# Kernel tuning notes

Measured on AMD Instinct MI355X. Metric: run time of the kernel, lower is better.

## Reference

```python
import jax, jax.numpy as jnp
import numpy as np

HIDDEN = 128
HEADS = 8
HEAD_DIM = HIDDEN // HEADS  # 16
N_NODE_TYPES = 3
N_EDGE_TYPES = 5
N_SRC = 50000
N_DST = 50000
N_EDGES = 800000
SCALE = float(np.sqrt(HEAD_DIM))


def setup_inputs() -> dict:
    key = jax.random.key(0)
    ks = jax.random.split(key, 12)
    lim = 1.0 / np.sqrt(HIDDEN)  # torch Linear default init range
    # xavier_uniform for [H, d, d] relation tensors: gain*sqrt(6/(fan_in+fan_out))
    xav = float(np.sqrt(6.0 / (HEAD_DIM + HEAD_DIM)))
    return {
        "x_src": jax.random.normal(ks[0], (N_SRC, HIDDEN), jnp.float32),
        "x_dst": jax.random.normal(ks[1], (N_DST, HIDDEN), jnp.float32),
        "edge_index": jax.random.randint(ks[2], (2, N_EDGES), 0, N_DST),
        "src_type": 0,
        "edge_type": 1,
        "dst_type": 2,
        "k_w": jax.random.uniform(ks[3], (N_NODE_TYPES, HIDDEN, HIDDEN), jnp.float32, -lim, lim),
        "k_b": jax.random.uniform(ks[4], (N_NODE_TYPES, HIDDEN), jnp.float32, -lim, lim),
        "q_w": jax.random.uniform(ks[5], (N_NODE_TYPES, HIDDEN, HIDDEN), jnp.float32, -lim, lim),
        "q_b": jax.random.uniform(ks[6], (N_NODE_TYPES, HIDDEN), jnp.float32, -lim, lim),
        "v_w": jax.random.uniform(ks[7], (N_NODE_TYPES, HIDDEN, HIDDEN), jnp.float32, -lim, lim),
        "v_b": jax.random.uniform(ks[8], (N_NODE_TYPES, HIDDEN), jnp.float32, -lim, lim),
        "relation_att": jax.random.uniform(ks[9], (N_EDGE_TYPES, HEADS, HEAD_DIM, HEAD_DIM), jnp.float32, -xav, xav),
        "relation_msg": jax.random.uniform(ks[10], (N_EDGE_TYPES, HEADS, HEAD_DIM, HEAD_DIM), jnp.float32, -xav, xav),
        "relation_pri": jnp.ones((N_EDGE_TYPES, HEADS), jnp.float32),
    }


def reference(x_src, x_dst, edge_index, src_type, edge_type, dst_type,
              k_w, k_b, q_w, q_b, v_w, v_b,
              relation_att, relation_msg, relation_pri):
    n_dst = x_dst.shape[0]
    # relation-specific node projections (torch Linear: x @ W.T + b)
    k = (x_src @ k_w[src_type].T + k_b[src_type]).reshape(-1, HEADS, HEAD_DIM)
    v = (x_src @ v_w[src_type].T + v_b[src_type]).reshape(-1, HEADS, HEAD_DIM)
    q = (x_dst @ q_w[dst_type].T + q_b[dst_type]).reshape(-1, HEADS, HEAD_DIM)

    src_idx, dst_idx = edge_index[0], edge_index[1]
    # gather + per-edge relation matmul: [E, H, d]
    k_edge = jnp.einsum('ehi,hio->eho', k[src_idx], relation_att[edge_type])
    att = (k_edge * q[dst_idx]).sum(-1) / SCALE + relation_pri[edge_type][None, :]  # [E, H]

    # segmented softmax over incoming edges per dst node.
    # torch scatter_reduce amax starts from a zero-initialized buffer -> max(0, seg_max)
    seg_max = jnp.maximum(jax.ops.segment_max(att, dst_idx, num_segments=n_dst), 0.0)
    att_exp = jnp.exp(att - seg_max[dst_idx])
    seg_sum = jnp.maximum(jax.ops.segment_sum(att_exp, dst_idx, num_segments=n_dst), 1e-8)
    att_n = att_exp / seg_sum[dst_idx]  # [E, H]

    # messages + weighted scatter-add aggregation
    msg = jnp.einsum('ehi,hio->eho', v[src_idx], relation_msg[edge_type])  # [E, H, d]
    out = jax.ops.segment_sum(att_n[..., None] * msg, dst_idx, num_segments=n_dst)
    return out.reshape(n_dst, HIDDEN)
```

## Files before the change

### kernel.cpp

```cpp
#include <hip/hip_runtime.h>

#define HIDDEN 128
#define HEADS 8
#define HDIM 16
#define BW 64

typedef unsigned int uint;
typedef unsigned short ushort;
typedef __attribute__((ext_vector_type(8))) short bfrag;
typedef __attribute__((ext_vector_type(4))) float f32x4;

__device__ inline ushort f2bf(float f) {
    uint u = __float_as_uint(f);
    uint r = ((u >> 16) & 1u) + 0x7fffu;
    return (ushort)((u + r) >> 16);
}
__device__ inline float bf2f(ushort h) { return __uint_as_float((uint)h << 16); }
__device__ inline float bfl(uint u) { return __uint_as_float(u << 16); }
__device__ inline float bfh(uint u) { return __uint_as_float(u & 0xffff0000u); }

__device__ inline int frag_addr(int k, int n) {
    int ks = k >> 5, kr = k & 31, nt = n >> 4;
    int lane = ((kr >> 3) << 4) | (n & 15);
    return ((ks * 8 + nt) * 64 + lane) * 8 + (kr & 7);
}

__global__ void k1a_weights_zero(
    const float* __restrict__ k_w, const float* __restrict__ k_b,
    const float* __restrict__ q_w, const float* __restrict__ q_b,
    const float* __restrict__ v_w, const float* __restrict__ v_b,
    const float* __restrict__ r_att, const float* __restrict__ r_msg,
    const int* __restrict__ stp, const int* __restrict__ etp, const int* __restrict__ dtp,
    ushort* __restrict__ WkHi, ushort* __restrict__ WvHi, ushort* __restrict__ WqHi,
    float* __restrict__ bk, float* __restrict__ bv, float* __restrict__ bq,
    int* __restrict__ deg, int n_dst)
{
    int idx = blockIdx.x * 256 + threadIdx.x;
    for (int i = idx; i < n_dst; i += 64 * 256) deg[i] = 0;

    int st = stp[0], et = etp[0], dt = dtp[0];
    int c = idx >> 7, j = idx & 127;
    int h = j >> 4, o = j & 15;
    const float* kw = k_w + (size_t)st * HIDDEN * HIDDEN;
    const float* vw = v_w + (size_t)st * HIDDEN * HIDDEN;
    const float* ra = r_att + (size_t)et * HEADS * HDIM * HDIM + h * HDIM * HDIM + o;
    const float* rm = r_msg + (size_t)et * HEADS * HDIM * HDIM + h * HDIM * HDIM + o;
    float sk = 0.f, sv = 0.f;
#pragma unroll
    for (int i = 0; i < HDIM; ++i) {
        sk += kw[(h * HDIM + i) * HIDDEN + c] * ra[i * HDIM];
        sv += vw[(h * HDIM + i) * HIDDEN + c] * rm[i * HDIM];
    }
    float sq = q_w[(size_t)dt * HIDDEN * HIDDEN + (size_t)j * HIDDEN + c];
    int fa = frag_addr(c, j);
    WkHi[fa] = f2bf(sk);
    WvHi[fa] = f2bf(sv);
    WqHi[fa] = f2bf(sq);
    if (idx < HIDDEN) {
        float sb = 0.f, sbv = 0.f;
#pragma unroll
        for (int i = 0; i < HDIM; ++i) {
            sb  += k_b[st * HIDDEN + h * HDIM + i] * ra[i * HDIM];
            sbv += v_b[st * HIDDEN + h * HDIM + i] * rm[i * HDIM];
        }
        bk[idx] = sb;
        bv[idx] = sbv;
        bq[idx] = q_b[dt * HIDDEN + idx];
    }
}

__global__ __launch_bounds__(256, 5) void k1b_proj_countfill(
    const float* __restrict__ x_src, const float* __restrict__ x_dst,
    const ushort* __restrict__ WkHi, const ushort* __restrict__ WvHi,
    const ushort* __restrict__ WqHi,
    const float* __restrict__ bk, const float* __restrict__ bv,
    const float* __restrict__ bq,
    ushort* __restrict__ kr16, ushort* __restrict__ vm16,
    float* __restrict__ qout, int n_src, int n_dst, int nsb, int nprojb,
    const int* __restrict__ ei, int* __restrict__ deg,
    ushort* __restrict__ bucket, int n_edges, int nfb)
{
    __shared__ float xs[32 * 132];
    int blk = blockIdx.x;

    if ((blk % 5) == 4) {
        int fidx = blk / 5;
        if (fidx >= nfb) return;
        int t = fidx * 256 + threadIdx.x;
        int base = t * 4;
        if (base >= n_edges) return;
        if (base + 3 < n_edges) {
            int4 ss = *(const int4*)(ei + base);
            int4 dd = *(const int4*)(ei + n_edges + base);
            int r0 = atomicAdd(&deg[dd.x], 1); if (r0 < BW) bucket[(size_t)dd.x * BW + r0] = (ushort)ss.x;
            int r1 = atomicAdd(&deg[dd.y], 1); if (r1 < BW) bucket[(size_t)dd.y * BW + r1] = (ushort)ss.y;
            int r2 = atomicAdd(&deg[dd.z], 1); if (r2 < BW) bucket[(size_t)dd.z * BW + r2] = (ushort)ss.z;
            int r3 = atomicAdd(&deg[dd.w], 1); if (r3 < BW) bucket[(size_t)dd.w * BW + r3] = (ushort)ss.w;
        } else {
            for (int e = base; e < n_edges; ++e) {
                int d = ei[n_edges + e];
                int r = atomicAdd(&deg[d], 1);
                if (r < BW) bucket[(size_t)d * BW + r] = (ushort)ei[e];
            }
        }
        return;
    }

    int pidx = blk - blk / 5;
    if (pidx >= nprojb) return;
    int is_src = (pidx < nsb) ? 1 : 0;
    int brow0 = (is_src ? pidx : pidx - nsb) * 32;
    int n = is_src ? n_src : n_dst;
    const float* x = is_src ? x_src : x_dst;
    int t = threadIdx.x;

    {
        const float4* xg = (const float4*)x;
#pragma unroll
        for (int k = 0; k < 4; ++k) {
            int fi = t + k * 256;
            int r = fi >> 5, c4 = fi & 31;
            int row = brow0 + r;
            float4 v = xg[(size_t)(row < n ? row : n - 1) * 32 + c4];
            *(float4*)&xs[r * 132 + c4 * 4] = v;
        }
    }
    __syncthreads();

    int w = t >> 6, l = t & 63;
    int l15 = l & 15, kgrp = l >> 4;
    int nthalf = w & 1;
    int rtile = w >> 1;
    int rowbase = brow0 + rtile * 16;

    bfrag ahi[4];
#pragma unroll
    for (int ks = 0; ks < 4; ++ks) {
        const float* xr = &xs[(rtile * 16 + l15) * 132 + ks * 32 + kgrp * 8];
        float4 x0 = *(const float4*)xr;
        float4 x1 = *(const float4*)(xr + 4);
        float xv[8] = {x0.x, x0.y, x0.z, x0.w, x1.x, x1.y, x1.z, x1.w};
#pragma unroll
        for (int b = 0; b < 8; ++b) {
            ahi[ks][b] = (short)f2bf(xv[b]);
        }
    }

    if (is_src) {
        const bfrag* Fk = (const bfrag*)WkHi;
        const bfrag* Fv = (const bfrag*)WvHi;
#pragma unroll
        for (int nt4 = 0; nt4 < 4; ++nt4) {
            int nt = nthalf * 4 + nt4;
            f32x4 ak = (f32x4){0.f, 0.f, 0.f, 0.f};
            f32x4 av = (f32x4){0.f, 0.f, 0.f, 0.f};
#pragma unroll
            for (int ks = 0; ks < 4; ++ks) {
                int fi = (ks * 8 + nt) * 64 + l;
                bfrag wk = Fk[fi], wv = Fv[fi];
                ak = __builtin_amdgcn_mfma_f32_16x16x32_bf16(ahi[ks], wk, ak, 0, 0, 0);
                av = __builtin_amdgcn_mfma_f32_16x16x32_bf16(ahi[ks], wv, av, 0, 0, 0);
            }
            int col = nt * 16 + l15;
            float bkc = bk[col], bvc = bv[col];
#pragma unroll
            for (int r = 0; r < 4; ++r) {
                int row = rowbase + kgrp * 4 + r;
                if (row < n) {
                    kr16[(size_t)row * HIDDEN + col] = f2bf(ak[r] + bkc);
                    vm16[(size_t)row * HIDDEN + col] = f2bf(av[r] + bvc);
                }
            }
        }
    } else {
        const bfrag* Fq = (const bfrag*)WqHi;
#pragma unroll
        for (int nt4 = 0; nt4 < 4; ++nt4) {
            int nt = nthalf * 4 + nt4;
            f32x4 aq = (f32x4){0.f, 0.f, 0.f, 0.f};
#pragma unroll
            for (int ks = 0; ks < 4; ++ks) {
                int fi = (ks * 8 + nt) * 64 + l;
                bfrag wq = Fq[fi];
                aq = __builtin_amdgcn_mfma_f32_16x16x32_bf16(ahi[ks], wq, aq, 0, 0, 0);
            }
            int col = nt * 16 + l15;
            float bqc = bq[col];
#pragma unroll
            for (int r = 0; r < 4; ++r) {
                int row = rowbase + kgrp * 4 + r;
                if (row < n) qout[(size_t)row * HIDDEN + col] = aq[r] + bqc;
            }
        }
    }
}

__global__ void fused_gather_kernel(const ushort* __restrict__ kr16,
                                    const ushort* __restrict__ vm16,
                                    const float* __restrict__ q,
                                    const float* __restrict__ pri,
                                    const int* __restrict__ etp,
                                    const int* __restrict__ deg,
                                    const ushort* __restrict__ bucket,
                                    float* __restrict__ out, int n_dst)
{
    int wave = (int)((blockIdx.x * 256 + threadIdx.x) >> 6);
    int l = threadIdx.x & 63;
    if (wave >= n_dst) return;
    int d = wave;
    int h = l >> 3;
    int e = l & 7;
    int len = deg[d]; if (len > BW) len = BW;
    const ushort* buck = bucket + (size_t)d * BW;

    const float4* qp = (const float4*)(q + (size_t)d * HIDDEN + h * HDIM);
    float4 q0 = qp[0], q1 = qp[1], q2 = qp[2], q3 = qp[3];
    float prih = pri[etp[0] * HEADS + h];

    float m = 0.0f;
    float ssum = 0.0f;
    float accx = 0.0f, accy = 0.0f;

    for (int i0 = 0; i0 < len; i0 += 16) {
        int ieA = i0 + e, ieB = i0 + 8 + e;
        bool vA = ieA < len, vB = ieB < len;
        int sA = buck[vA ? ieA : 0];
        int sB = buck[vB ? ieB : 0];

        const uint4* kpA = (const uint4*)(kr16 + (size_t)sA * HIDDEN + h * HDIM);
        const uint4* kpB = (const uint4*)(kr16 + (size_t)sB * HIDDEN + h * HDIM);
        uint4 kaA = kpA[0], kbA = kpA[1];
        uint4 kaB = kpB[0], kbB = kpB[1];

        float dotA =
            bfl(kaA.x) * q0.x + bfh(kaA.x) * q0.y + bfl(kaA.y) * q0.z + bfh(kaA.y) * q0.w +
            bfl(kaA.z) * q1.x + bfh(kaA.z) * q1.y + bfl(kaA.w) * q1.z + bfh(kaA.w) * q1.w +
            bfl(kbA.x) * q2.x + bfh(kbA.x) * q2.y + bfl(kbA.y) * q2.z + bfh(kbA.y) * q2.w +
            bfl(kbA.z) * q3.x + bfh(kbA.z) * q3.y + bfl(kbA.w) * q3.z + bfh(kbA.w) * q3.w;
        float dotB =
            bfl(kaB.x) * q0.x + bfh(kaB.x) * q0.y + bfl(kaB.y) * q0.z + bfh(kaB.y) * q0.w +
            bfl(kaB.z) * q1.x + bfh(kaB.z) * q1.y + bfl(kaB.w) * q1.z + bfh(kaB.w) * q1.w +
            bfl(kbB.x) * q2.x + bfh(kbB.x) * q2.y + bfl(kbB.y) * q2.z + bfh(kbB.y) * q2.w +
            bfl(kbB.z) * q3.x + bfh(kbB.z) * q3.y + bfl(kbB.w) * q3.z + bfh(kbB.w) * q3.w;

        float aA = vA ? (dotA * 0.25f + prih) : -3.0e38f;
        float aB = vB ? (dotB * 0.25f + prih) : -3.0e38f;

        float pm = fmaxf(aA, aB);
        pm = fmaxf(pm, __shfl_xor(pm, 1));
        pm = fmaxf(pm, __shfl_xor(pm, 2));
        pm = fmaxf(pm, __shfl_xor(pm, 4));
        float mnew = fmaxf(m, pm);
        float c = __expf(m - mnew);
        float wA = vA ? __expf(aA - mnew) : 0.0f;
        float wB = vB ? __expf(aB - mnew) : 0.0f;
        float S = wA + wB;
        S += __shfl_xor(S, 1);
        S += __shfl_xor(S, 2);
        S += __shfl_xor(S, 4);
        ssum = ssum * c + S;
        accx *= c;
        accy *= c;
        m = mnew;

#pragma unroll
        for (int ee = 0; ee < 8; ++ee) {
            int se = __shfl(sA, ee);
            float we = __shfl(wA, (l & 56) | ee);
            uint vv = *(const uint*)(vm16 + (size_t)se * HIDDEN + 2 * l);
            accx += we * bfl(vv);
            accy += we * bfh(vv);
        }
        if (i0 + 8 < len) {
#pragma unroll
            for (int ee = 0; ee < 8; ++ee) {
                int se = __shfl(sB, ee);
                float we = __shfl(wB, (l & 56) | ee);
                uint vv = *(const uint*)(vm16 + (size_t)se * HIDDEN + 2 * l);
                accx += we * bfl(vv);
                accy += we * bfh(vv);
            }
        }
    }

    float inv = 1.0f / fmaxf(ssum, 1e-8f);
    float2 o; o.x = accx * inv; o.y = accy * inv;
    *(float2*)(out + (size_t)d * HIDDEN + 2 * l) = o;
}

extern "C" void kernel_launch(void* const* d_in, const int* in_sizes, int n_in,
                              void* d_out, int out_size, void* d_ws, size_t ws_size,
                              hipStream_t stream)
{
    const float* x_src = (const float*)d_in[0];
    const float* x_dst = (const float*)d_in[1];
    const int*   ei    = (const int*)d_in[2];
    const int*   stp   = (const int*)d_in[3];
    const int*   etp   = (const int*)d_in[4];
    const int*   dtp   = (const int*)d_in[5];
    const float* k_w   = (const float*)d_in[6];
    const float* k_b   = (const float*)d_in[7];
    const float* q_w   = (const float*)d_in[8];
    const float* q_b   = (const float*)d_in[9];
    const float* v_w   = (const float*)d_in[10];
    const float* v_b   = (const float*)d_in[11];
    const float* r_att = (const float*)d_in[12];
    const float* r_msg = (const float*)d_in[13];
    const float* r_pri = (const float*)d_in[14];

    int n_src   = in_sizes[0] / HIDDEN;
    int n_dst   = in_sizes[1] / HIDDEN;
    int n_edges = in_sizes[2] / 2;
    float* out = (float*)d_out;

    char* p = (char*)d_ws;
    ushort* kr16 = (ushort*)p;            p += (size_t)n_src * HIDDEN * sizeof(ushort);
    ushort* vm16 = (ushort*)p;            p += (size_t)n_src * HIDDEN * sizeof(ushort);
    float*  qv   = (float*)p;             p += (size_t)n_dst * HIDDEN * sizeof(float);
    ushort* bucket = (ushort*)p;          p += (size_t)n_dst * BW * sizeof(ushort);
    int* deg     = (int*)p;               p += (size_t)n_dst * sizeof(int);
    float* bk = (float*)p;                p += HIDDEN * sizeof(float);
    float* bv = (float*)p;                p += HIDDEN * sizeof(float);
    float* bq = (float*)p;                p += HIDDEN * sizeof(float);
    ushort* WkHi = (ushort*)p;            p += HIDDEN * HIDDEN * sizeof(ushort);
    ushort* WvHi = (ushort*)p;            p += HIDDEN * HIDDEN * sizeof(ushort);
    ushort* WqHi = (ushort*)p;            p += HIDDEN * HIDDEN * sizeof(ushort);

    k1a_weights_zero<<<64, 256, 0, stream>>>(
        k_w, k_b, q_w, q_b, v_w, v_b, r_att, r_msg, stp, etp, dtp,
        WkHi, WvHi, WqHi, bk, bv, bq, deg, n_dst);

    int nsb = (n_src + 31) / 32;
    int ndb = (n_dst + 31) / 32;
    int nprojb = nsb + ndb;
    int nfb = (n_edges / 4 + 256) / 256;
    int grid1 = 5 * nfb;
    int grid2 = ((nprojb + 3) / 4) * 5;
    int grid = grid1 > grid2 ? grid1 : grid2;
    k1b_proj_countfill<<<grid, 256, 0, stream>>>(
        x_src, x_dst, WkHi, WvHi, WqHi, bk, bv, bq,
        kr16, vm16, qv, n_src, n_dst, nsb, nprojb,
        ei, deg, bucket, n_edges, nfb);

    fused_gather_kernel<<<(int)(((size_t)n_dst * 64 + 255) / 256), 256, 0, stream>>>(
        kr16, vm16, qv, r_pri, etp, deg, bucket, out, n_dst);
}
```

Baseline: 128.4 us.

## Process two destination nodes per wave and rebalance edge-fill interleaving

The gather kernel now has each wavefront handle two destination nodes at once, interleaving their key and value gathers so more independent memory loads are in flight per wave. The grid is halved to match. Separately, the projection/count-fill kernel switches from a 4:1 projection-to-fill block interleave with four edges per thread to a 1:1 interleave with one edge per thread. The aim is to hide gather latency and spread the atomic fill work more evenly, at the cost of more registers per thread, lower occupancy, and wasted iterations when the two nodes have different degrees.

```diff
diff --git a/kernel.cpp b/kernel.cpp
--- a/kernel.cpp
+++ b/kernel.cpp
@@ -83,30 +83,19 @@
     __shared__ float xs[32 * 132];
     int blk = blockIdx.x;
 
-    if ((blk % 5) == 4) {
-        int fidx = blk / 5;
+    if (blk & 1) {
+        int fidx = blk >> 1;
         if (fidx >= nfb) return;
-        int t = fidx * 256 + threadIdx.x;
-        int base = t * 4;
-        if (base >= n_edges) return;
-        if (base + 3 < n_edges) {
-            int4 ss = *(const int4*)(ei + base);
-            int4 dd = *(const int4*)(ei + n_edges + base);
-            int r0 = atomicAdd(&deg[dd.x], 1); if (r0 < BW) bucket[(size_t)dd.x * BW + r0] = (ushort)ss.x;
-            int r1 = atomicAdd(&deg[dd.y], 1); if (r1 < BW) bucket[(size_t)dd.y * BW + r1] = (ushort)ss.y;
-            int r2 = atomicAdd(&deg[dd.z], 1); if (r2 < BW) bucket[(size_t)dd.z * BW + r2] = (ushort)ss.z;
-            int r3 = atomicAdd(&deg[dd.w], 1); if (r3 < BW) bucket[(size_t)dd.w * BW + r3] = (ushort)ss.w;
-        } else {
-            for (int e = base; e < n_edges; ++e) {
-                int d = ei[n_edges + e];
-                int r = atomicAdd(&deg[d], 1);
-                if (r < BW) bucket[(size_t)d * BW + r] = (ushort)ei[e];
-            }
-        }
+        int e = fidx * 256 + threadIdx.x;
+        if (e >= n_edges) return;
+        int s = ei[e];
+        int d = ei[n_edges + e];
+        int r = atomicAdd(&deg[d], 1);
+        if (r < BW) bucket[(size_t)d * BW + r] = (ushort)s;
         return;
     }
 
-    int pidx = blk - blk / 5;
+    int pidx = blk >> 1;
     if (pidx >= nprojb) return;
     int is_src = (pidx < nsb) ? 1 : 0;
     int brow0 = (is_src ? pidx : pidx - nsb) * 32;
@@ -206,86 +195,162 @@
 {
     int wave = (int)((blockIdx.x * 256 + threadIdx.x) >> 6);
     int l = threadIdx.x & 63;
-    if (wave >= n_dst) return;
-    int d = wave;
+    int d0 = wave * 2;
+    if (d0 >= n_dst) return;
+    int d1 = d0 + 1;
+    bool has1 = d1 < n_dst;
     int h = l >> 3;
     int e = l & 7;
-    int len = deg[d]; if (len > BW) len = BW;
-    const ushort* buck = bucket + (size_t)d * BW;
-
-    const float4* qp = (const float4*)(q + (size_t)d * HIDDEN + h * HDIM);
-    float4 q0 = qp[0], q1 = qp[1], q2 = qp[2], q3 = qp[3];
+
+    int len0 = deg[d0]; if (len0 > BW) len0 = BW;
+    int len1 = has1 ? deg[d1] : 0; if (len1 > BW) len1 = BW;
+    const ushort* buck0 = bucket + (size_t)d0 * BW;
+    const ushort* buck1 = bucket + (size_t)d1 * BW;
+
+    const float4* qp0 = (const float4*)(q + (size_t)d0 * HIDDEN + h * HDIM);
+    float4 q00 = qp0[0], q01 = qp0[1], q02 = qp0[2], q03 = qp0[3];
+    const float4* qp1 = (const float4*)(q + (size_t)(has1 ? d1 : d0) * HIDDEN + h * HDIM);
+    float4 q10 = qp1[0], q11 = qp1[1], q12 = qp1[2], q13 = qp1[3];
+
     float prih = pri[etp[0] * HEADS + h];
 
-    float m = 0.0f;
-    float ssum = 0.0f;
-    float accx = 0.0f, accy = 0.0f;
-
-    for (int i0 = 0; i0 < len; i0 += 16) {
+    float m0 = 0.0f, ss0 = 0.0f, ax0 = 0.0f, ay0 = 0.0f;
+    float m1 = 0.0f, ss1 = 0.0f, ax1 = 0.0f, ay1 = 0.0f;
+
+    int lenmax = len0 > len1 ? len0 : len1;
+    for (int i0 = 0; i0 < lenmax; i0 += 16) {
         int ieA = i0 + e, ieB = i0 + 8 + e;
-        bool vA = ieA < len, vB = ieB < len;
-        int sA = buck[vA ? ieA : 0];
-        int sB = buck[vB ? ieB : 0];
-
-        const uint4* kpA = (const uint4*)(kr16 + (size_t)sA * HIDDEN + h * HDIM);
-        const uint4* kpB = (const uint4*)(kr16 + (size_t)sB * HIDDEN + h * HDIM);
-        uint4 kaA = kpA[0], kbA = kpA[1];
-        uint4 kaB = kpB[0], kbB = kpB[1];
-
-        float dotA =
-            bfl(kaA.x) * q0.x + bfh(kaA.x) * q0.y + bfl(kaA.y) * q0.z + bfh(kaA.y) * q0.w +
-            bfl(kaA.z) * q1.x + bfh(kaA.z) * q1.y + bfl(kaA.w) * q1.z + bfh(kaA.w) * q1.w +
-            bfl(kbA.x) * q2.x + bfh(kbA.x) * q2.y + bfl(kbA.y) * q2.z + bfh(kbA.y) * q2.w +
-            bfl(kbA.z) * q3.x + bfh(kbA.z) * q3.y + bfl(kbA.w) * q3.z + bfh(kbA.w) * q3.w;
-        float dotB =
-            bfl(kaB.x) * q0.x + bfh(kaB.x) * q0.y + bfl(kaB.y) * q0.z + bfh(kaB.y) * q0.w +
-            bfl(kaB.z) * q1.x + bfh(kaB.z) * q1.y + bfl(kaB.w) * q1.z + bfh(kaB.w) * q1.w +
-            bfl(kbB.x) * q2.x + bfh(kbB.x) * q2.y + bfl(kbB.y) * q2.z + bfh(kbB.y) * q2.w +
-            bfl(kbB.z) * q3.x + bfh(kbB.z) * q3.y + bfl(kbB.w) * q3.z + bfh(kbB.w) * q3.w;
-
-        float aA = vA ? (dotA * 0.25f + prih) : -3.0e38f;
-        float aB = vB ? (dotB * 0.25f + prih) : -3.0e38f;
-
-        float pm = fmaxf(aA, aB);
-        pm = fmaxf(pm, __shfl_xor(pm, 1));
-        pm = fmaxf(pm, __shfl_xor(pm, 2));
-        pm = fmaxf(pm, __shfl_xor(pm, 4));
-        float mnew = fmaxf(m, pm);
-        float c = __expf(m - mnew);
-        float wA = vA ? __expf(aA - mnew) : 0.0f;
-        float wB = vB ? __expf(aB - mnew) : 0.0f;
-        float S = wA + wB;
-        S += __shfl_xor(S, 1);
-        S += __shfl_xor(S, 2);
-        S += __shfl_xor(S, 4);
-        ssum = ssum * c + S;
-        accx *= c;
-        accy *= c;
-        m = mnew;
-
-#pragma unroll
-        for (int ee = 0; ee < 8; ++ee) {
-            int se = __shfl(sA, ee);
-            float we = __shfl(wA, (l & 56) | ee);
-            uint vv = *(const uint*)(vm16 + (size_t)se * HIDDEN + 2 * l);
-            accx += we * bfl(vv);
-            accy += we * bfh(vv);
-        }
-        if (i0 + 8 < len) {
-#pragma unroll
-            for (int ee = 0; ee < 8; ++ee) {
-                int se = __shfl(sB, ee);
-                float we = __shfl(wB, (l & 56) | ee);
-                uint vv = *(const uint*)(vm16 + (size_t)se * HIDDEN + 2 * l);
-                accx += we * bfl(vv);
-                accy += we * bfh(vv);
-            }
-        }
-    }
-
-    float inv = 1.0f / fmaxf(ssum, 1e-8f);
-    float2 o; o.x = accx * inv; o.y = accy * inv;
-    *(float2*)(out + (size_t)d * HIDDEN + 2 * l) = o;
+        bool vA0 = ieA < len0, vB0 = ieB < len0;
+        bool vA1 = ieA < len1, vB1 = ieB < len1;
+        int sA0 = vA0 ? (int)buck0[ieA] : 0;
+        int sB0 = vB0 ? (int)buck0[ieB] : 0;
+        int sA1 = vA1 ? (int)buck1[ieA] : 0;
+        int sB1 = vB1 ? (int)buck1[ieB] : 0;
+
+        const uint4* kpA0 = (const uint4*)(kr16 + (size_t)sA0 * HIDDEN + h * HDIM);
+        const uint4* kpB0 = (const uint4*)(kr16 + (size_t)sB0 * HIDDEN + h * HDIM);
+        const uint4* kpA1 = (const uint4*)(kr16 + (size_t)sA1 * HIDDEN + h * HDIM);
+        const uint4* kpB1 = (const uint4*)(kr16 + (size_t)sB1 * HIDDEN + h * HDIM);
+        uint4 a0a = kpA0[0], a0b = kpA0[1];
+        uint4 b0a = kpB0[0], b0b = kpB0[1];
+        uint4 a1a = kpA1[0], a1b = kpA1[1];
+        uint4 b1a = kpB1[0], b1b = kpB1[1];
+
+        {
+            float dotA =
+                bfl(a0a.x) * q00.x + bfh(a0a.x) * q00.y + bfl(a0a.y) * q00.z + bfh(a0a.y) * q00.w +
+                bfl(a0a.z) * q01.x + bfh(a0a.z) * q01.y + bfl(a0a.w) * q01.z + bfh(a0a.w) * q01.w +
+                bfl(a0b.x) * q02.x + bfh(a0b.x) * q02.y + bfl(a0b.y) * q02.z + bfh(a0b.y) * q02.w +
+                bfl(a0b.z) * q03.x + bfh(a0b.z) * q03.y + bfl(a0b.w) * q03.z + bfh(a0b.w) * q03.w;
+            float dotB =
+                bfl(b0a.x) * q00.x + bfh(b0a.x) * q00.y + bfl(b0a.y) * q00.z + bfh(b0a.y) * q00.w +
+                bfl(b0a.z) * q01.x + bfh(b0a.z) * q01.y + bfl(b0a.w) * q01.z + bfh(b0a.w) * q01.w +
+                bfl(b0b.x) * q02.x + bfh(b0b.x) * q02.y + bfl(b0b.y) * q02.z + bfh(b0b.y) * q02.w +
+                bfl(b0b.z) * q03.x + bfh(b0b.z) * q03.y + bfl(b0b.w) * q03.z + bfh(b0b.w) * q03.w;
+            float aA = vA0 ? (dotA * 0.25f + prih) : -3.0e38f;
+            float aB = vB0 ? (dotB * 0.25f + prih) : -3.0e38f;
+            float pm = fmaxf(aA, aB);
+            pm = fmaxf(pm, __shfl_xor(pm, 1));
+            pm = fmaxf(pm, __shfl_xor(pm, 2));
+            pm = fmaxf(pm, __shfl_xor(pm, 4));
+            float mnew = fmaxf(m0, pm);
+            float c = __expf(m0 - mnew);
+            float wA = vA0 ? __expf(aA - mnew) : 0.0f;
+            float wB = vB0 ? __expf(aB - mnew) : 0.0f;
+            float S = wA + wB;
+            S += __shfl_xor(S, 1);
+            S += __shfl_xor(S, 2);
+            S += __shfl_xor(S, 4);
+            ss0 = ss0 * c + S;
+            ax0 *= c;
+            ay0 *= c;
+            m0 = mnew;
+
+            if (i0 < len0) {
+#pragma unroll
+                for (int ee = 0; ee < 8; ++ee) {
+                    int se = __shfl(sA0, ee);
+                    float we = __shfl(wA, (l & 56) | ee);
+                    uint vv = *(const uint*)(vm16 + (size_t)se * HIDDEN + 2 * l);
+                    ax0 += we * bfl(vv);
+                    ay0 += we * bfh(vv);
+                }
+            }
+            if (i0 + 8 < len0) {
+#pragma unroll
+                for (int ee = 0; ee < 8; ++ee) {
+                    int se = __shfl(sB0, ee);
+                    float we = __shfl(wB, (l & 56) | ee);
+                    uint vv = *(const uint*)(vm16 + (size_t)se * HIDDEN + 2 * l);
+                    ax0 += we * bfl(vv);
+                    ay0 += we * bfh(vv);
+                }
+            }
+        }
+
+        {
+            float dotA =
+                bfl(a1a.x) * q10.x + bfh(a1a.x) * q10.y + bfl(a1a.y) * q10.z + bfh(a1a.y) * q10.w +
+                bfl(a1a.z) * q11.x + bfh(a1a.z) * q11.y + bfl(a1a.w) * q11.z + bfh(a1a.w) * q11.w +
+                bfl(a1b.x) * q12.x + bfh(a1b.x) * q12.y + bfl(a1b.y) * q12.z + bfh(a1b.y) * q12.w +
+                bfl(a1b.z) * q13.x + bfh(a1b.z) * q13.y + bfl(a1b.w) * q13.z + bfh(a1b.w) * q13.w;
+            float dotB =
+                bfl(b1a.x) * q10.x + bfh(b1a.x) * q10.y + bfl(b1a.y) * q10.z + bfh(b1a.y) * q10.w +
+                bfl(b1a.z) * q11.x + bfh(b1a.z) * q11.y + bfl(b1a.w) * q11.z + bfh(b1a.w) * q11.w +
+                bfl(b1b.x) * q12.x + bfh(b1b.x) * q12.y + bfl(b1b.y) * q12.z + bfh(b1b.y) * q12.w +
+                bfl(b1b.z) * q13.x + bfh(b1b.z) * q13.y + bfl(b1b.w) * q13.z + bfh(b1b.w) * q13.w;
+            float aA = vA1 ? (dotA * 0.25f + prih) : -3.0e38f;
+            float aB = vB1 ? (dotB * 0.25f + prih) : -3.0e38f;
+            float pm = fmaxf(aA, aB);
+            pm = fmaxf(pm, __shfl_xor(pm, 1));
+            pm = fmaxf(pm, __shfl_xor(pm, 2));
+            pm = fmaxf(pm, __shfl_xor(pm, 4));
+            float mnew = fmaxf(m1, pm);
+            float c = __expf(m1 - mnew);
+            float wA = vA1 ? __expf(aA - mnew) : 0.0f;
+            float wB = vB1 ? __expf(aB - mnew) : 0.0f;
+            float S = wA + wB;
+            S += __shfl_xor(S, 1);
+            S += __shfl_xor(S, 2);
+            S += __shfl_xor(S, 4);
+            ss1 = ss1 * c + S;
+            ax1 *= c;
+            ay1 *= c;
+            m1 = mnew;
+
+            if (i0 < len1) {
+#pragma unroll
+                for (int ee = 0; ee < 8; ++ee) {
+                    int se = __shfl(sA1, ee);
+                    float we = __shfl(wA, (l & 56) | ee);
+                    uint vv = *(const uint*)(vm16 + (size_t)se * HIDDEN + 2 * l);
+                    ax1 += we * bfl(vv);
+                    ay1 += we * bfh(vv);
+                }
+            }
+            if (i0 + 8 < len1) {
+#pragma unroll
+                for (int ee = 0; ee < 8; ++ee) {
+                    int se = __shfl(sB1, ee);
+                    float we = __shfl(wB, (l & 56) | ee);
+                    uint vv = *(const uint*)(vm16 + (size_t)se * HIDDEN + 2 * l);
+                    ax1 += we * bfl(vv);
+                    ay1 += we * bfh(vv);
+                }
+            }
+        }
+    }
+
+    {
+        float inv = 1.0f / fmaxf(ss0, 1e-8f);
+        float2 o; o.x = ax0 * inv; o.y = ay0 * inv;
+        *(float2*)(out + (size_t)d0 * HIDDEN + 2 * l) = o;
+    }
+    if (has1) {
+        float inv = 1.0f / fmaxf(ss1, 1e-8f);
+        float2 o; o.x = ax1 * inv; o.y = ay1 * inv;
+        *(float2*)(out + (size_t)d1 * HIDDEN + 2 * l) = o;
+    }
 }
 
 extern "C" void kernel_launch(void* const* d_in, const int* in_sizes, int n_in,
@@ -333,15 +398,14 @@
     int nsb = (n_src + 31) / 32;
     int ndb = (n_dst + 31) / 32;
     int nprojb = nsb + ndb;
-    int nfb = (n_edges / 4 + 256) / 256;
-    int grid1 = 5 * nfb;
-    int grid2 = ((nprojb + 3) / 4) * 5;
-    int grid = grid1 > grid2 ? grid1 : grid2;
-    k1b_proj_countfill<<<grid, 256, 0, stream>>>(
+    int nfb = (n_edges + 255) / 256;
+    int bigger = nprojb > nfb ? nprojb : nfb;
+    k1b_proj_countfill<<<2 * bigger, 256, 0, stream>>>(
         x_src, x_dst, WkHi, WvHi, WqHi, bk, bv, bq,
         kr16, vm16, qv, n_src, n_dst, nsb, nprojb,
         ei, deg, bucket, n_edges, nfb);
 
-    fused_gather_kernel<<<(int)(((size_t)n_dst * 64 + 255) / 256), 256, 0, stream>>>(
+    int nwaves = (n_dst + 1) / 2;
+    fused_gather_kernel<<<(int)(((size_t)nwaves * 64 + 255) / 256), 256, 0, stream>>>(
         kr16, vm16, qv, r_pri, etp, deg, bucket, out, n_dst);
 }
```

Measured after the change: 152.6 us. +18.8%, slower.

## Interleave count-fill blocks 1:1 with projection and prefetch V rows early

Applied to the files above, without the earlier changes.

The fused projection/bucket-fill kernel now alternates projection and edge-bucketing blocks one-to-one, and each fill thread handles a single edge instead of four, spreading the atomics over more blocks. In the gather kernel, all sixteen V-row loads for a chunk are issued before the softmax math so their latency overlaps the dot products and reductions. The cost is more registers held per thread in the gather loop and a larger launch grid in the first kernel.

```diff
diff --git a/kernel.cpp b/kernel.cpp
--- a/kernel.cpp
+++ b/kernel.cpp
@@ -83,30 +83,19 @@
     __shared__ float xs[32 * 132];
     int blk = blockIdx.x;
 
-    if ((blk % 5) == 4) {
-        int fidx = blk / 5;
+    if (blk & 1) {
+        int fidx = blk >> 1;
         if (fidx >= nfb) return;
-        int t = fidx * 256 + threadIdx.x;
-        int base = t * 4;
-        if (base >= n_edges) return;
-        if (base + 3 < n_edges) {
-            int4 ss = *(const int4*)(ei + base);
-            int4 dd = *(const int4*)(ei + n_edges + base);
-            int r0 = atomicAdd(&deg[dd.x], 1); if (r0 < BW) bucket[(size_t)dd.x * BW + r0] = (ushort)ss.x;
-            int r1 = atomicAdd(&deg[dd.y], 1); if (r1 < BW) bucket[(size_t)dd.y * BW + r1] = (ushort)ss.y;
-            int r2 = atomicAdd(&deg[dd.z], 1); if (r2 < BW) bucket[(size_t)dd.z * BW + r2] = (ushort)ss.z;
-            int r3 = atomicAdd(&deg[dd.w], 1); if (r3 < BW) bucket[(size_t)dd.w * BW + r3] = (ushort)ss.w;
-        } else {
-            for (int e = base; e < n_edges; ++e) {
-                int d = ei[n_edges + e];
-                int r = atomicAdd(&deg[d], 1);
-                if (r < BW) bucket[(size_t)d * BW + r] = (ushort)ei[e];
-            }
-        }
+        int e = fidx * 256 + threadIdx.x;
+        if (e >= n_edges) return;
+        int s = ei[e];
+        int d = ei[n_edges + e];
+        int r = atomicAdd(&deg[d], 1);
+        if (r < BW) bucket[(size_t)d * BW + r] = (ushort)s;
         return;
     }
 
-    int pidx = blk - blk / 5;
+    int pidx = blk >> 1;
     if (pidx >= nprojb) return;
     int is_src = (pidx < nsb) ? 1 : 0;
     int brow0 = (is_src ? pidx : pidx - nsb) * 32;
@@ -224,6 +213,7 @@
     for (int i0 = 0; i0 < len; i0 += 16) {
         int ieA = i0 + e, ieB = i0 + 8 + e;
         bool vA = ieA < len, vB = ieB < len;
+        bool useB = (i0 + 8) < len;
         int sA = buck[vA ? ieA : 0];
         int sB = buck[vB ? ieB : 0];
 
@@ -231,6 +221,20 @@
         const uint4* kpB = (const uint4*)(kr16 + (size_t)sB * HIDDEN + h * HDIM);
         uint4 kaA = kpA[0], kbA = kpA[1];
         uint4 kaB = kpB[0], kbB = kpB[1];
+
+        uint vvA[8], vvB[8];
+#pragma unroll
+        for (int ee = 0; ee < 8; ++ee) {
+            int se = __shfl(sA, ee);
+            vvA[ee] = *(const uint*)(vm16 + (size_t)se * HIDDEN + 2 * l);
+        }
+        if (useB) {
+#pragma unroll
+            for (int ee = 0; ee < 8; ++ee) {
+                int se = __shfl(sB, ee);
+                vvB[ee] = *(const uint*)(vm16 + (size_t)se * HIDDEN + 2 * l);
+            }
+        }
 
         float dotA =
             bfl(kaA.x) * q0.x + bfh(kaA.x) * q0.y + bfl(kaA.y) * q0.z + bfh(kaA.y) * q0.w +
@@ -265,20 +269,16 @@
 
 #pragma unroll
         for (int ee = 0; ee < 8; ++ee) {
-            int se = __shfl(sA, ee);
             float we = __shfl(wA, (l & 56) | ee);
-            uint vv = *(const uint*)(vm16 + (size_t)se * HIDDEN + 2 * l);
-            accx += we * bfl(vv);
-            accy += we * bfh(vv);
-        }
-        if (i0 + 8 < len) {
+            accx += we * bfl(vvA[ee]);
+            accy += we * bfh(vvA[ee]);
+        }
+        if (useB) {
 #pragma unroll
             for (int ee = 0; ee < 8; ++ee) {
-                int se = __shfl(sB, ee);
                 float we = __shfl(wB, (l & 56) | ee);
-                uint vv = *(const uint*)(vm16 + (size_t)se * HIDDEN + 2 * l);
-                accx += we * bfl(vv);
-                accy += we * bfh(vv);
+                accx += we * bfl(vvB[ee]);
+                accy += we * bfh(vvB[ee]);
             }
         }
     }
@@ -333,11 +333,9 @@
     int nsb = (n_src + 31) / 32;
     int ndb = (n_dst + 31) / 32;
     int nprojb = nsb + ndb;
-    int nfb = (n_edges / 4 + 256) / 256;
-    int grid1 = 5 * nfb;
-    int grid2 = ((nprojb + 3) / 4) * 5;
-    int grid = grid1 > grid2 ? grid1 : grid2;
-    k1b_proj_countfill<<<grid, 256, 0, stream>>>(
+    int nfb = (n_edges + 255) / 256;
+    int bigger = nprojb > nfb ? nprojb : nfb;
+    k1b_proj_countfill<<<2 * bigger, 256, 0, stream>>>(
         x_src, x_dst, WkHi, WvHi, WqHi, bk, bv, bq,
         kr16, vm16, qv, n_src, n_dst, nsb, nprojb,
         ei, deg, bucket, n_edges, nfb);
```

Measured after the change: 128.4 us. No clear change (-0.0%).
